# Kernel tuning notes

Hardware: AMD Instinct MI355X
Metric: run time of the kernel (lower is better)

The kernel has to match this reference:

```python
import jax, jax.numpy as jnp
import numpy as np

D = 512      # encoder_dim
DI = 1024    # mamba d_inner = expand * d_model
N = 16       # d_state
DTR = 32     # dt_rank = ceil(512/16)
K = 4        # d_conv
B, L = 8, 512


def _ln(x, g, b, eps=1e-5):
    m = jnp.mean(x, -1, keepdims=True)
    v = jnp.mean((x - m) ** 2, -1, keepdims=True)
    return (x - m) / jnp.sqrt(v + eps) * g + b


def _silu(x):
    return x * jax.nn.sigmoid(x)


def _ffn(x, g, b, w1, b1, w2, b2):
    h = _ln(x, g, b)
    h = _silu(h @ w1.T + b1)
    return h @ w2.T + b2


def _dwconv(x, w, pl, pr):
    # x: (B,C,L); w: (C,K) depthwise kernel
    return jax.lax.conv_general_dilated(
        x, w[:, None, :], (1,), [(pl, pr)],
        feature_group_count=x.shape[1], dimension_numbers=('NCH', 'OIH', 'NCH'))


def _mamba(x, win, convw, convb, wx, wdt, bdt, Alog, Dp, wout):
    b = x.shape[0]
    xz = jnp.einsum('bld,ed->ble', x, win)            # (B,L,2*DI)
    xi, z = jnp.split(xz, 2, -1)
    xc = _dwconv(xi.transpose(0, 2, 1), convw, K - 1, 0) + convb[None, :, None]
    xc = _silu(xc).transpose(0, 2, 1)                 # (B,L,DI) causal conv + silu
    xdb = jnp.einsum('bld,ed->ble', xc, wx)           # (B,L,DTR+2N)
    dt, Bm, Cm = xdb[..., :DTR], xdb[..., DTR:DTR + N], xdb[..., DTR + N:]
    dt = jax.nn.softplus(jnp.einsum('blr,dr->bld', dt, wdt) + bdt)
    A = -jnp.exp(Alog)                                # (DI,N)
    dA = jnp.exp(dt[..., None] * A)                   # (B,L,DI,N)
    dBx = dt[..., None] * Bm[:, :, None, :] * xc[..., None]

    def step(h, t):
        dA_t, dBx_t, C_t = t
        h = dA_t * h + dBx_t
        return h, jnp.einsum('bdn,bn->bd', h, C_t)

    h0 = jnp.zeros((b, DI, N), x.dtype)
    _, ys = jax.lax.scan(step, h0, (dA.transpose(1, 0, 2, 3),
                                    dBx.transpose(1, 0, 2, 3),
                                    Cm.transpose(1, 0, 2)))
    y = ys.transpose(1, 0, 2) + Dp * xc
    y = y * _silu(z)
    return jnp.einsum('bld,od->blo', y, wout)


def _bimamba(x, m_win, m_convw, m_convb, m_wx, m_wdt, m_bdt, m_Alog, m_D, m_wout, bi_wo, bi_bo):
    f = _mamba(x, m_win[0], m_convw[0], m_convb[0], m_wx[0], m_wdt[0], m_bdt[0],
               m_Alog[0], m_D[0], m_wout[0])
    r = _mamba(x[:, ::-1], m_win[1], m_convw[1], m_convb[1], m_wx[1], m_wdt[1], m_bdt[1],
               m_Alog[1], m_D[1], m_wout[1])
    cat = jnp.concatenate([f, r[:, ::-1]], -1)
    return cat @ bi_wo.T + bi_bo


def _convmod(x, ln_g, ln_b, pw1_w, pw1_b, dw15, dw31, dw63,
             bn_g, bn_b, bn_m, bn_v, pw2_w, pw2_b):
    h = _ln(x, ln_g, ln_b).transpose(0, 2, 1)          # (B,D,L)
    h = jnp.einsum('bcl,oc->bol', h, pw1_w) + pw1_b[None, :, None]
    a, g = jnp.split(h, 2, 1)
    h = a * jax.nn.sigmoid(g)                          # GLU on channel dim
    outs = [_dwconv(h, w, (w.shape[-1] - 1) // 2, (w.shape[-1] - 1) // 2)
            for w in (dw15, dw31, dw63)]
    out = (outs[0] + outs[1] + outs[2]) / 3.0          # merge_mode='avg'
    out = (out - bn_m[None, :, None]) / jnp.sqrt(bn_v[None, :, None] + 1e-5) \
          * bn_g[None, :, None] + bn_b[None, :, None]
    out = _silu(out)
    out = jnp.einsum('bcl,oc->bol', out, pw2_w) + pw2_b[None, :, None]
    return out.transpose(0, 2, 1)


def setup_inputs() -> dict:
    key = jax.random.key(0)
    ks = iter(jax.random.split(key, 64))
    def w(*shape, s=0.02):
        return jax.random.normal(next(ks), shape, jnp.float32) * s
    inp = {}
    inp['x'] = jax.random.normal(next(ks), (B, L, D), jnp.float32)
    for p in ('ff1', 'ff2'):
        inp[p + '_ln_g'] = jnp.ones((D,), jnp.float32)
        inp[p + '_ln_b'] = jnp.zeros((D,), jnp.float32)
        inp[p + '_w1'] = w(4 * D, D)
        inp[p + '_b1'] = jnp.zeros((4 * D,), jnp.float32)
        inp[p + '_w2'] = w(D, 4 * D)
        inp[p + '_b2'] = jnp.zeros((D,), jnp.float32)
    inp['m_win'] = w(2, 2 * DI, D)
    inp['m_convw'] = w(2, DI, K, s=0.1)
    inp['m_convb'] = jnp.zeros((2, DI), jnp.float32)
    inp['m_wx'] = w(2, DTR + 2 * N, DI)
    inp['m_wdt'] = w(2, DI, DTR, s=0.1)
    inp['m_bdt'] = jnp.full((2, DI), float(np.log(np.expm1(0.01))), jnp.float32)
    inp['m_Alog'] = jnp.log(jnp.tile(jnp.arange(1, N + 1, dtype=jnp.float32), (2, DI, 1)))
    inp['m_D'] = jnp.ones((2, DI), jnp.float32)
    inp['m_wout'] = w(2, D, DI)
    inp['bi_wo'] = w(D, 2 * D)
    inp['bi_bo'] = jnp.zeros((D,), jnp.float32)
    inp['cv_ln_g'] = jnp.ones((D,), jnp.float32)
    inp['cv_ln_b'] = jnp.zeros((D,), jnp.float32)
    inp['cv_pw1_w'] = w(2 * D, D)
    inp['cv_pw1_b'] = jnp.zeros((2 * D,), jnp.float32)
    inp['cv_dw15'] = w(D, 15, s=0.1)
    inp['cv_dw31'] = w(D, 31, s=0.1)
    inp['cv_dw63'] = w(D, 63, s=0.1)
    inp['cv_bn_g'] = jnp.ones((D,), jnp.float32)
    inp['cv_bn_b'] = jnp.zeros((D,), jnp.float32)
    inp['cv_bn_m'] = jnp.zeros((D,), jnp.float32)
    inp['cv_bn_v'] = jnp.ones((D,), jnp.float32)
    inp['cv_pw2_w'] = w(D, D)
    inp['cv_pw2_b'] = jnp.zeros((D,), jnp.float32)
    inp['ln_g'] = jnp.ones((D,), jnp.float32)
    inp['ln_b'] = jnp.zeros((D,), jnp.float32)
    return inp


def reference(x, ff1_ln_g, ff1_ln_b, ff1_w1, ff1_b1, ff1_w2, ff1_b2,
              ff2_ln_g, ff2_ln_b, ff2_w1, ff2_b1, ff2_w2, ff2_b2,
              m_win, m_convw, m_convb, m_wx, m_wdt, m_bdt, m_Alog, m_D, m_wout,
              bi_wo, bi_bo,
              cv_ln_g, cv_ln_b, cv_pw1_w, cv_pw1_b, cv_dw15, cv_dw31, cv_dw63,
              cv_bn_g, cv_bn_b, cv_bn_m, cv_bn_v, cv_pw2_w, cv_pw2_b,
              ln_g, ln_b):
    h = x + 0.5 * _ffn(x, ff1_ln_g, ff1_ln_b, ff1_w1, ff1_b1, ff1_w2, ff1_b2)
    h = h + _bimamba(h, m_win, m_convw, m_convb, m_wx, m_wdt, m_bdt,
                     m_Alog, m_D, m_wout, bi_wo, bi_bo)
    h = h + _convmod(h, cv_ln_g, cv_ln_b, cv_pw1_w, cv_pw1_b, cv_dw15, cv_dw31, cv_dw63,
                     cv_bn_g, cv_bn_b, cv_bn_m, cv_bn_v, cv_pw2_w, cv_pw2_b)
    h = h + 0.5 * _ffn(h, ff2_ln_g, ff2_ln_b, ff2_w1, ff2_b1, ff2_w2, ff2_b2)
    return _ln(h, ln_g, ln_b)
```

## Files before the change

kernel.cpp:

```cpp
#include <hip/hip_runtime.h>
#include <hip/hip_bf16.h>
#include <math.h>

#define LL   512
#define DD   512
#define DII  1024
#define NST  16
#define BB   8
#define MM   4096
#define CHL  32
#define NCH  16
#define MB_  (1024*1024)
#define Q_(n) ((size_t)(n)*262144)

typedef __attribute__((ext_vector_type(8))) short bf16x8;
typedef __attribute__((ext_vector_type(4))) float f32x4;

__device__ __forceinline__ float fast_rcp(float x){ return __builtin_amdgcn_rcpf(x); }
__device__ __forceinline__ float sigmoidf_(float x){ return fast_rcp(1.0f + __expf(-x)); }
__device__ __forceinline__ float siluf_(float x){ return x * sigmoidf_(x); }
__device__ __forceinline__ float softplusf_(float x){
    return fmaxf(x, 0.0f) + __logf(1.0f + __expf(-fabsf(x)));
}

__device__ __forceinline__ short f2bf(float f) {
    union { float f; unsigned u; } v; v.f = f;
    unsigned r = v.u + 0x7fffu + ((v.u >> 16) & 1u);
    return (short)(r >> 16);
}
__device__ __forceinline__ float bf2f(short s) {
    union { unsigned u; float f; } v; v.u = ((unsigned)(unsigned short)s) << 16;
    return v.f;
}
__device__ __forceinline__ bf16x8 pack_bf8(float4 v0, float4 v1) {
    union { bf16x8 v; short e[8]; } pk;
    pk.e[0]=f2bf(v0.x); pk.e[1]=f2bf(v0.y); pk.e[2]=f2bf(v0.z); pk.e[3]=f2bf(v0.w);
    pk.e[4]=f2bf(v1.x); pk.e[5]=f2bf(v1.y); pk.e[6]=f2bf(v1.z); pk.e[7]=f2bf(v1.w);
    return pk.v;
}
__device__ __forceinline__ void gl_lds16(const short* g, short* l) {
    __builtin_amdgcn_global_load_lds(
        (const __attribute__((address_space(1))) void*)g,
        (__attribute__((address_space(3))) void*)l, 16, 0, 0);
}

struct WcvtArgs { const float* s[10]; short* d[10]; int n[10]; };
__global__ void __launch_bounds__(256) wcvt_kernel(WcvtArgs a) {
    const int seg = blockIdx.y;
    const int i = (blockIdx.x*256 + threadIdx.x) * 8;
    if (i >= a.n[seg]) return;
    const float* s = a.s[seg] + i;
    float4 v0 = *(const float4*)s;
    float4 v1 = *(const float4*)(s + 4);
    int di = i;
    if (seg == 8) di = ((i >> 5) << 6) | (i & 31);
    *(bf16x8*)(a.d[seg] + di) = pack_bf8(v0, v1);
}

__global__ void __launch_bounds__(256) woutT_kernel(
    const float* __restrict__ wout, short* __restrict__ outT)
{
    __shared__ float sh[64][65];
    const int o0 = blockIdx.x << 6;
    const int j0 = blockIdx.y << 6;
    const int d  = blockIdx.z;
    const float* in = wout + (size_t)d*512*1024;
    short* out = outT + (size_t)d*1024*512;
    const int t = threadIdx.x;
    const int c4 = (t & 15) << 2;
    const int r  = t >> 4;
    #pragma unroll
    for (int i = 0; i < 4; i++) {
        int orow = r + i*16;
        float4 v = *(const float4*)(in + (size_t)(o0 + orow)*1024 + j0 + c4);
        sh[orow][c4+0]=v.x; sh[orow][c4+1]=v.y; sh[orow][c4+2]=v.z; sh[orow][c4+3]=v.w;
    }
    __syncthreads();
    #pragma unroll
    for (int i = 0; i < 4; i++) {
        int jr = r + i*16;
        short4 o;
        o.x = f2bf(sh[c4+0][jr]); o.y = f2bf(sh[c4+1][jr]);
        o.z = f2bf(sh[c4+2][jr]); o.w = f2bf(sh[c4+3][jr]);
        *(short4*)(out + (size_t)(j0 + jr)*512 + o0 + c4) = o;
    }
}

__global__ void __launch_bounds__(512) gemm9_kernel(
    const short* __restrict__ A, int lda,
    const short* __restrict__ W, int ldw,
    const float* __restrict__ bias,
    short* __restrict__ outB, int ldc,
    int kLen, int act)
{
    __shared__ short As[3][128*64];
    __shared__ short Ws[3][256*64];

    const int tid = threadIdx.x, lane = tid & 63, wid = tid >> 6;

    int nwg = gridDim.x * gridDim.y;
    int flat = blockIdx.y * gridDim.x + blockIdx.x;
    if (!(nwg & 7)) { int cpx = nwg >> 3; flat = (flat & 7)*cpx + (flat >> 3); }
    const int bx = flat % gridDim.x, by = flat / gridDim.x;
    const int rowBase = by << 7;
    const int colBase = bx << 8;

    size_t asrc[2];
    #pragma unroll
    for (int rd = 0; rd < 2; rd++) {
        int id = rd*512 + tid, row = id >> 3, u = id & 7;
        asrc[rd] = (size_t)(rowBase + row)*lda + ((u ^ (row & 7)) << 3);
    }
    size_t wsrc[4];
    #pragma unroll
    for (int rd = 0; rd < 4; rd++) {
        int id = rd*512 + tid, row = id >> 3, u = id & 7;
        wsrc[rd] = (size_t)(colBase + row)*ldw + ((u ^ (row & 7)) << 3);
    }

    const int fr = lane & 15;
    const int swz0 = ((((lane >> 4)    ) ^ (lane & 7)) << 3);
    const int swz1 = ((((lane >> 4) | 4) ^ (lane & 7)) << 3);
    const int wm = (wid >> 2) * 64, wn = (wid & 3) * 64;

    f32x4 acc[4][4] = {};

    auto STAGE = [&](int buf, int k0) {
        #pragma unroll
        for (int rd = 0; rd < 2; rd++)
            gl_lds16(A + asrc[rd] + k0, &As[buf][(rd*512 + tid)*8]);
        #pragma unroll
        for (int rd = 0; rd < 4; rd++)
            gl_lds16(W + wsrc[rd] + k0, &Ws[buf][(rd*512 + tid)*8]);
    };

    const int nT = kLen >> 6;
    STAGE(0, 0);
    if (nT > 1) STAGE(1, 64);
    for (int t = 0; t < nT; ++t) {
        if (t + 2 < nT) {
            STAGE((t+2)%3, (t+2)*64);
            asm volatile("s_waitcnt vmcnt(12)" ::: "memory");
        } else if (t + 1 < nT) {
            asm volatile("s_waitcnt vmcnt(6)" ::: "memory");
        } else {
            asm volatile("s_waitcnt vmcnt(0)" ::: "memory");
        }
        __builtin_amdgcn_sched_barrier(0);
        __builtin_amdgcn_s_barrier();
        __builtin_amdgcn_sched_barrier(0);
        const int cur = t % 3;
        #pragma unroll
        for (int ks = 0; ks < 2; ks++) {
            const int so = ks ? swz1 : swz0;
            bf16x8 af[4], bfr[4];
            #pragma unroll
            for (int mi = 0; mi < 4; mi++)
                af[mi] = *(const bf16x8*)&As[cur][(wm + mi*16 + fr)*64 + so];
            #pragma unroll
            for (int ni = 0; ni < 4; ni++)
                bfr[ni] = *(const bf16x8*)&Ws[cur][(wn + ni*16 + fr)*64 + so];
            #pragma unroll
            for (int mi = 0; mi < 4; mi++)
                #pragma unroll
                for (int ni = 0; ni < 4; ni++)
                    acc[mi][ni] = __builtin_amdgcn_mfma_f32_16x16x32_bf16(af[mi], bfr[ni], acc[mi][ni], 0, 0, 0);
        }
        __builtin_amdgcn_sched_barrier(0);
        __builtin_amdgcn_s_barrier();
        __builtin_amdgcn_sched_barrier(0);
    }

    #pragma unroll
    for (int mi = 0; mi < 4; mi++)
        #pragma unroll
        for (int r = 0; r < 4; r++) {
            int orow = rowBase + wm + mi*16 + ((lane>>4)<<2) + r;
            #pragma unroll
            for (int ni = 0; ni < 4; ni++) {
                int gcol = colBase + wn + ni*16 + fr;
                float v = acc[mi][ni][r];
                if (bias) v += bias[gcol];
                if (act == 1) v = siluf_(v);
                outB[(size_t)orow*ldc + gcol] = f2bf(v);
            }
        }
}

template<int BN>
__global__ void __launch_bounds__(256) gemm3_kernel(
    const short* __restrict__ A, int lda,
    const short* __restrict__ W, int ldw,
    const float* __restrict__ bias,
    float* __restrict__ outF, short* __restrict__ outB, int ldc,
    int kLen, int kOff, int act, int actLim,
    size_t zA, size_t zW, int zB, size_t zO, int rowsPerW,
    float* __restrict__ partial, size_t pstride, int N)
{
    constexpr int WN = BN / 64;
    constexpr int WM = 4 / WN;
    constexpr int TM = 64 / WM;
    constexpr int FM = TM / 16;
    constexpr int WRW = BN / 32;

    __shared__ short As[2][64*64];
    __shared__ short Ws[2][BN*64];

    const int tid = threadIdx.x, lane = tid & 63, wid = tid >> 6;
    const int z = blockIdx.z;
    A += (size_t)z * zA;
    if (outF) outF += (size_t)z * zO;
    if (outB) outB += (size_t)z * zO;

    int nwg = gridDim.x * gridDim.y;
    int flat = blockIdx.y * gridDim.x + blockIdx.x;
    if (!(nwg & 7)) { int cpx = nwg >> 3; flat = (flat & 7)*cpx + (flat >> 3); }
    const int bx = flat % gridDim.x, by = flat / gridDim.x;

    const int rowBase = by << 6;
    const int colBase = bx * BN;
    const int kBase = z * kOff;

    const int dsel = rowsPerW ? (rowBase / rowsPerW) : z;
    W += (size_t)dsel * zW;
    if (bias) bias += (size_t)dsel * (size_t)zB;

    size_t asrc[2];
    #pragma unroll
    for (int rd = 0; rd < 2; rd++) {
        int id = rd*256 + tid, row = id >> 3, u = id & 7;
        asrc[rd] = (size_t)(rowBase + row)*lda + ((u ^ (row & 7)) << 3);
    }
    size_t wsrc[WRW];
    #pragma unroll
    for (int rd = 0; rd < WRW; rd++) {
        int id = rd*256 + tid, row = id >> 3, u = id & 7;
        wsrc[rd] = (size_t)(colBase + row)*ldw + ((u ^ (row & 7)) << 3);
    }

    const int fr = lane & 15;
    const int swz0 = ((((lane >> 4)    ) ^ (lane & 7)) << 3);
    const int swz1 = ((((lane >> 4) | 4) ^ (lane & 7)) << 3);
    const int wm = (wid / WN) * TM, wn = (wid % WN) * 64;

    f32x4 acc[FM][4] = {};

    auto STAGE = [&](int buf, int k0) {
        #pragma unroll
        for (int rd = 0; rd < 2; rd++)
            gl_lds16(A + asrc[rd] + k0, &As[buf][(rd*256 + tid)*8]);
        #pragma unroll
        for (int rd = 0; rd < WRW; rd++)
            gl_lds16(W + wsrc[rd] + k0, &Ws[buf][(rd*256 + tid)*8]);
    };

    const int nT = kLen >> 6;
    STAGE(0, kBase);
    int cur = 0;
    for (int t = 0; t < nT; ++t) {
        if (t + 1 < nT) {
            STAGE(cur ^ 1, kBase + (t+1)*64);
            asm volatile("s_waitcnt vmcnt(6)" ::: "memory");
        } else {
            asm volatile("s_waitcnt vmcnt(0)" ::: "memory");
        }
        __builtin_amdgcn_sched_barrier(0);
        __builtin_amdgcn_s_barrier();
        __builtin_amdgcn_sched_barrier(0);
        #pragma unroll
        for (int ks = 0; ks < 2; ks++) {
            const int so = ks ? swz1 : swz0;
            bf16x8 af[FM], bfr[4];
            #pragma unroll
            for (int mi = 0; mi < FM; mi++)
                af[mi] = *(const bf16x8*)&As[cur][(wm + mi*16 + fr)*64 + so];
            #pragma unroll
            for (int ni = 0; ni < 4; ni++)
                bfr[ni] = *(const bf16x8*)&Ws[cur][(wn + ni*16 + fr)*64 + so];
            #pragma unroll
            for (int mi = 0; mi < FM; mi++)
                #pragma unroll
                for (int ni = 0; ni < 4; ni++)
                    acc[mi][ni] = __builtin_amdgcn_mfma_f32_16x16x32_bf16(af[mi], bfr[ni], acc[mi][ni], 0, 0, 0);
        }
        __builtin_amdgcn_sched_barrier(0);
        __builtin_amdgcn_s_barrier();
        __builtin_amdgcn_sched_barrier(0);
        cur ^= 1;
    }

    if (partial) {
        float* pp = partial + (size_t)z * pstride;
        #pragma unroll
        for (int mi = 0; mi < FM; mi++)
            #pragma unroll
            for (int r = 0; r < 4; r++) {
                int orow = rowBase + wm + mi*16 + ((lane>>4)<<2) + r;
                #pragma unroll
                for (int ni = 0; ni < 4; ni++)
                    pp[(size_t)orow*N + colBase + wn + ni*16 + fr] = acc[mi][ni][r];
            }
    } else {
        #pragma unroll
        for (int mi = 0; mi < FM; mi++)
            #pragma unroll
            for (int r = 0; r < 4; r++) {
                int orow = rowBase + wm + mi*16 + ((lane>>4)<<2) + r;
                #pragma unroll
                for (int ni = 0; ni < 4; ni++) {
                    int gcol = colBase + wn + ni*16 + fr;
                    float v = acc[mi][ni][r];
                    if (bias) v += bias[gcol];
                    if (gcol < actLim) {
                        if (act == 1) v = siluf_(v);
                        else if (act == 2) v = softplusf_(v);
                    }
                    if (outF) outF[(size_t)orow*ldc + gcol] = v;
                    if (outB) outB[(size_t)orow*ldc + gcol] = f2bf(v);
                }
            }
    }
}

__global__ void __launch_bounds__(256) reduce_kernel(
    const float* __restrict__ part, int S, size_t pstride, int N,
    short* __restrict__ outB, int ldc)
{
    const int i4 = blockIdx.x*256 + threadIdx.x;
    const int row = i4 / (N >> 2);
    const int c4  = (i4 - row*(N >> 2)) << 2;
    float4 s = *(const float4*)(part + (size_t)row*N + c4);
    for (int z = 1; z < S; z++) {
        float4 t = *(const float4*)(part + (size_t)z*pstride + (size_t)row*N + c4);
        s.x += t.x; s.y += t.y; s.z += t.z; s.w += t.w;
    }
    short4 o; o.x=f2bf(s.x); o.y=f2bf(s.y); o.z=f2bf(s.z); o.w=f2bf(s.w);
    *(short4*)(outB + (size_t)row*ldc + c4) = o;
}

__global__ void __launch_bounds__(128) redln_kernel(
    const float* __restrict__ part, int S,
    const float* __restrict__ bias,
    const float* __restrict__ resid, float rscale,
    float* __restrict__ houtF, short* __restrict__ houtB,
    const float* __restrict__ lng, const float* __restrict__ lnb2,
    float* __restrict__ lnoutF, short* __restrict__ lnoutB)
{
    const int row = blockIdx.x;
    const int t = threadIdx.x;
    const size_t pstride = (size_t)MM*512;
    float4 s = ((const float4*)(part + (size_t)row*512))[t];
    for (int z = 1; z < S; z++) {
        float4 v = ((const float4*)(part + z*pstride + (size_t)row*512))[t];
        s.x += v.x; s.y += v.y; s.z += v.z; s.w += v.w;
    }
    if (bias) { float4 b = ((const float4*)bias)[t]; s.x+=b.x; s.y+=b.y; s.z+=b.z; s.w+=b.w; }
    if (resid) {
        float4 r = ((const float4*)(resid + (size_t)row*512))[t];
        s.x = r.x + rscale*s.x; s.y = r.y + rscale*s.y;
        s.z = r.z + rscale*s.z; s.w = r.w + rscale*s.w;
    }
    if (houtF) ((float4*)(houtF + (size_t)row*512))[t] = s;
    if (houtB) {
        short4 o; o.x=f2bf(s.x); o.y=f2bf(s.y); o.z=f2bf(s.z); o.w=f2bf(s.w);
        *(short4*)(houtB + (size_t)row*512 + t*4) = o;
    }
    if (!lng) return;
    float sum = s.x+s.y+s.z+s.w;
    float sq  = s.x*s.x+s.y*s.y+s.z*s.z+s.w*s.w;
    #pragma unroll
    for (int off = 32; off >= 1; off >>= 1) {
        sum += __shfl_down(sum, off);
        sq  += __shfl_down(sq, off);
    }
    __shared__ float sh[4];
    if ((t & 63) == 0) { sh[(t>>6)*2] = sum; sh[(t>>6)*2+1] = sq; }
    __syncthreads();
    float mean = (sh[0]+sh[2]) * (1.0f/512.f);
    float var  = (sh[1]+sh[3]) * (1.0f/512.f) - mean*mean;
    float rstd = rsqrtf(var + 1e-5f);
    float4 gg = ((const float4*)lng)[t];
    float4 bb = ((const float4*)lnb2)[t];
    float4 o;
    o.x = (s.x-mean)*rstd*gg.x + bb.x;
    o.y = (s.y-mean)*rstd*gg.y + bb.y;
    o.z = (s.z-mean)*rstd*gg.z + bb.z;
    o.w = (s.w-mean)*rstd*gg.w + bb.w;
    if (lnoutF) ((float4*)(lnoutF + (size_t)row*512))[t] = o;
    if (lnoutB) {
        short4 ob; ob.x=f2bf(o.x); ob.y=f2bf(o.y); ob.z=f2bf(o.z); ob.w=f2bf(o.w);
        *(short4*)(lnoutB + (size_t)row*512 + t*4) = ob;
    }
}

__global__ void __launch_bounds__(128) ln_kernel(
    const float* __restrict__ x, const float* __restrict__ g,
    const float* __restrict__ bta, short* __restrict__ outB)
{
    const int row = blockIdx.x;
    const int t = threadIdx.x;
    float4 v = ((const float4*)(x + (size_t)row*DD))[t];
    float s = v.x+v.y+v.z+v.w;
    float q = v.x*v.x+v.y*v.y+v.z*v.z+v.w*v.w;
    #pragma unroll
    for (int off = 32; off >= 1; off >>= 1) {
        s += __shfl_down(s, off);
        q += __shfl_down(q, off);
    }
    __shared__ float sh[4];
    if ((t & 63) == 0) { sh[(t>>6)*2] = s; sh[(t>>6)*2+1] = q; }
    __syncthreads();
    float mean = (sh[0]+sh[2]) * (1.0f/DD);
    float var  = (sh[1]+sh[3]) * (1.0f/DD) - mean*mean;
    float rstd = rsqrtf(var + 1e-5f);
    float4 gg = ((const float4*)g)[t];
    float4 bb = ((const float4*)bta)[t];
    short4 ob;
    ob.x = f2bf((v.x-mean)*rstd*gg.x + bb.x);
    ob.y = f2bf((v.y-mean)*rstd*gg.y + bb.y);
    ob.z = f2bf((v.z-mean)*rstd*gg.z + bb.z);
    ob.w = f2bf((v.w-mean)*rstd*gg.w + bb.w);
    *(short4*)(outB + (size_t)row*DD + t*4) = ob;
}

__global__ void __launch_bounds__(256) conv_both_kernel(
    const short* __restrict__ xz_all, const float* __restrict__ cw,
    const float* __restrict__ cb, short* __restrict__ xc_both)
{
    const int gid = blockIdx.x*256 + threadIdx.x;
    const int c4  = (gid & 255) << 2;
    const int row = (gid >> 8) & (MM-1);
    const int dir = gid >> 20;
    const int l   = row & (LL-1);
    const short* base = xz_all + (size_t)(row - l)*4096 + dir*2048 + c4;
    float acc[4];
    #pragma unroll
    for (int j = 0; j < 4; j++) acc[j] = cb[dir*1024 + c4 + j];
    float wt[4][4];
    #pragma unroll
    for (int j = 0; j < 4; j++) {
        float4 w = *(const float4*)(cw + (size_t)dir*4096 + (c4 + j)*4);
        wt[j][0]=w.x; wt[j][1]=w.y; wt[j][2]=w.z; wt[j][3]=w.w;
    }
    #pragma unroll
    for (int t = 0; t < 4; t++) {
        int lt = dir ? (l + 3 - t) : (l - 3 + t);
        if (lt >= 0 && lt < LL) {
            short4 u = *(const short4*)(base + (size_t)lt*4096);
            acc[0] += wt[0][t]*bf2f(u.x);
            acc[1] += wt[1][t]*bf2f(u.y);
            acc[2] += wt[2][t]*bf2f(u.z);
            acc[3] += wt[3][t]*bf2f(u.w);
        }
    }
    short4 o;
    o.x = f2bf(siluf_(acc[0])); o.y = f2bf(siluf_(acc[1]));
    o.z = f2bf(siluf_(acc[2])); o.w = f2bf(siluf_(acc[3]));
    *(short4*)(xc_both + (size_t)dir*MM*1024 + (size_t)row*1024 + c4) = o;
}

__global__ void __launch_bounds__(256) scan_a_kernel(
    const short* __restrict__ dt_bf, const short* __restrict__ xc_both,
    const short* __restrict__ xdb_bf, const float* __restrict__ Alog,
    float* __restrict__ S_dt, short* __restrict__ H)
{
    const int bid = blockIdx.x;
    const int dg  = bid & 3;
    const int c   = (bid >> 2) & (NCH-1);
    const int b   = (bid >> 6) & 7;
    const int dir = bid >> 9;
    const int d   = (dg << 8) + threadIdx.x;

    float Aexp[16];
    #pragma unroll
    for (int n = 0; n < 16; n++) Aexp[n] = -__expf(Alog[dir*16384 + d*16 + n]);
    const float A0 = Aexp[0];
    int fast = 1;
    #pragma unroll
    for (int n = 1; n < 16; n++)
        fast &= (fabsf(Aexp[n] - (float)(n+1)*A0) <= 1e-4f*fabsf(Aexp[n]) + 1e-6f);

    float h[16];
    #pragma unroll
    for (int n = 0; n < 16; n++) h[n] = 0.f;
    float S = 0.f;

    const size_t rbase = (size_t)b*LL + (size_t)c*CHL;
    const short* dtp = dt_bf + ((size_t)dir*MM + rbase)*1024 + d;
    const short* bcp = xdb_bf + ((size_t)dir*MM + rbase)*64 + 32;
    const short* xcp = xc_both + ((size_t)dir*MM + rbase)*1024 + d;

#define SCAN_A_BODY(FASTQ) \
    for (int i = 0; i < CHL; i++) { \
        int lp = dir ? (CHL-1-i) : i; \
        float dtv = bf2f(dtp[(size_t)lp*1024]); \
        float xcv = bf2f(xcp[(size_t)lp*1024]); \
        S += dtv; \
        float co = dtv*xcv; \
        union { bf16x8 v; short e[8]; } b0, b1; \
        b0.v = *(const bf16x8*)(bcp + (size_t)lp*64); \
        b1.v = *(const bf16x8*)(bcp + (size_t)lp*64 + 8); \
        float q[16]; \
        if (FASTQ) { \
            float p = __expf(dtv*A0); float qq = p; \
            _Pragma("unroll") for (int n = 0; n < 16; n++) { q[n] = qq; qq *= p; } \
        } else { \
            _Pragma("unroll") for (int n = 0; n < 16; n++) q[n] = __expf(dtv*Aexp[n]); \
        } \
        _Pragma("unroll") for (int n = 0; n < 16; n++) { \
            float Bv = bf2f(n < 8 ? b0.e[n] : b1.e[n & 7]); \
            h[n] = fmaf(q[n], h[n], co*Bv); \
        } \
    }
    if (fast) { SCAN_A_BODY(1) } else { SCAN_A_BODY(0) }
#undef SCAN_A_BODY

    S_dt[(((size_t)dir*BB + b)*NCH + c)*1024 + d] = S;
    const size_t hb = ((((size_t)dir*BB + b)*NCH + c)*16)*1024 + d;
    #pragma unroll
    for (int n = 0; n < 16; n++) H[hb + (size_t)n*1024] = f2bf(h[n]);
}

__global__ void __launch_bounds__(256) scan_b_kernel(
    const float* __restrict__ S_dt, short* H, const float* __restrict__ Alog)
{
    const int g = blockIdx.x*256 + threadIdx.x;
    const int d = g & 1023;
    const int n = (g >> 10) & 15;
    const int b = (g >> 14) & 7;
    const int dir = g >> 17;
    const float Aexp = -__expf(Alog[dir*16384 + d*16 + n]);
    float h = 0.f;
    for (int ci = 0; ci < NCH; ci++) {
        int c = dir ? (NCH-1-ci) : ci;
        float S = S_dt[(((size_t)dir*BB + b)*NCH + c)*1024 + d];
        size_t i = ((((size_t)dir*BB + b)*NCH + c)*16 + n)*1024 + d;
        float q = __expf(Aexp*S);
        float hn = q*h + bf2f(H[i]);
        H[i] = f2bf(h);
        h = hn;
    }
}

__global__ void __launch_bounds__(256) scan_c_kernel(
    const short* __restrict__ dt_bf, short* xc_ys,
    const short* __restrict__ xdb_bf, const float* __restrict__ Alog,
    const short* __restrict__ H, const short* __restrict__ xz_all,
    const float* __restrict__ Dp)
{
    const int bid = blockIdx.x;
    const int dg  = bid & 3;
    const int c   = (bid >> 2) & (NCH-1);
    const int b   = (bid >> 6) & 7;
    const int dir = bid >> 9;
    const int d   = (dg << 8) + threadIdx.x;

    float Aexp[16];
    #pragma unroll
    for (int n = 0; n < 16; n++) Aexp[n] = -__expf(Alog[dir*16384 + d*16 + n]);
    const float A0 = Aexp[0];
    int fast = 1;
    #pragma unroll
    for (int n = 1; n < 16; n++)
        fast &= (fabsf(Aexp[n] - (float)(n+1)*A0) <= 1e-4f*fabsf(Aexp[n]) + 1e-6f);
    const float Dpv = Dp[dir*1024 + d];

    float h[16];
    const size_t hb = ((((size_t)dir*BB + b)*NCH + c)*16)*1024 + d;
    #pragma unroll
    for (int n = 0; n < 16; n++) h[n] = bf2f(H[hb + (size_t)n*1024]);

    const size_t rbase = (size_t)b*LL + (size_t)c*CHL;
    const short* dtp = dt_bf + ((size_t)dir*MM + rbase)*1024 + d;
    const short* bcp = xdb_bf + ((size_t)dir*MM + rbase)*64 + 32;
    short*       xcp = xc_ys + ((size_t)dir*MM + rbase)*1024 + d;
    const short* zp  = xz_all + rbase*4096 + dir*2048 + 1024 + d;

#define SCAN_C_BODY(FASTQ) \
    for (int i = 0; i < CHL; i++) { \
        int lp = dir ? (CHL-1-i) : i; \
        float dtv = bf2f(dtp[(size_t)lp*1024]); \
        float xcv = bf2f(xcp[(size_t)lp*1024]); \
        float zv  = bf2f(zp[(size_t)lp*4096]); \
        float co = dtv*xcv; \
        union { bf16x8 v; short e[8]; } b0, b1, c0, c1; \
        b0.v = *(const bf16x8*)(bcp + (size_t)lp*64); \
        b1.v = *(const bf16x8*)(bcp + (size_t)lp*64 + 8); \
        c0.v = *(const bf16x8*)(bcp + (size_t)lp*64 + 16); \
        c1.v = *(const bf16x8*)(bcp + (size_t)lp*64 + 24); \
        float q[16]; \
        if (FASTQ) { \
            float p = __expf(dtv*A0); float qq = p; \
            _Pragma("unroll") for (int n = 0; n < 16; n++) { q[n] = qq; qq *= p; } \
        } else { \
            _Pragma("unroll") for (int n = 0; n < 16; n++) q[n] = __expf(dtv*Aexp[n]); \
        } \
        float y = 0.f; \
        _Pragma("unroll") for (int n = 0; n < 16; n++) { \
            float Bv = bf2f(n < 8 ? b0.e[n] : b1.e[n & 7]); \
            float Cv = bf2f(n < 8 ? c0.e[n] : c1.e[n & 7]); \
            h[n] = fmaf(q[n], h[n], co*Bv); \
            y = fmaf(Cv, h[n], y); \
        } \
        float out = (y + Dpv*xcv) * siluf_(zv); \
        xcp[(size_t)lp*1024] = f2bf(out); \
    }
    if (fast) { SCAN_C_BODY(1) } else { SCAN_C_BODY(0) }
#undef SCAN_C_BODY
}

__global__ void __launch_bounds__(256) glu_transpose_kernel(
    const float* __restrict__ pw1, float* __restrict__ out_t)
{
    __shared__ float sh[64][65];
    const int c0 = blockIdx.x << 6;
    const int l0 = blockIdx.y << 6;
    const int b  = blockIdx.z;
    const int t  = threadIdx.x;
    const int c4 = (t & 15) << 2;
    const int r  = t >> 4;
    #pragma unroll
    for (int i = 0; i < 4; i++) {
        int lrow = r + i*16;
        size_t row = (size_t)(b << 9) + l0 + lrow;
        float4 a = *(const float4*)(pw1 + row*1024 + c0 + c4);
        float4 g = *(const float4*)(pw1 + row*1024 + 512 + c0 + c4);
        sh[lrow][c4+0] = a.x * sigmoidf_(g.x);
        sh[lrow][c4+1] = a.y * sigmoidf_(g.y);
        sh[lrow][c4+2] = a.z * sigmoidf_(g.z);
        sh[lrow][c4+3] = a.w * sigmoidf_(g.w);
    }
    __syncthreads();
    #pragma unroll
    for (int i = 0; i < 4; i++) {
        int crow = r + i*16;
        float4 o;
        o.x = sh[c4+0][crow];
        o.y = sh[c4+1][crow];
        o.z = sh[c4+2][crow];
        o.w = sh[c4+3][crow];
        *(float4*)(out_t + ((size_t)(b << 9) + c0 + crow)*512 + l0 + c4) = o;
    }
}

__global__ void __launch_bounds__(256) multiconv_t_kernel(
    const float* __restrict__ gin_t,
    const float* __restrict__ w15, const float* __restrict__ w31,
    const float* __restrict__ w63,
    const float* __restrict__ bn_g, const float* __restrict__ bn_b,
    const float* __restrict__ bn_m, const float* __restrict__ bn_v,
    float* __restrict__ out_t)
{
    __shared__ float sh[574];
    const int c = blockIdx.x & (DD-1);
    const int b = blockIdx.x >> 9;
    const int t = threadIdx.x;
    const float* rowp = gin_t + ((size_t)(b << 9) + c)*512;
    sh[31 + t]       = rowp[t];
    sh[31 + t + 256] = rowp[t + 256];
    if (t < 31) { sh[t] = 0.f; sh[543 + t] = 0.f; }
    __syncthreads();

    const float bnscale = rsqrtf(bn_v[c] + 1e-5f) * bn_g[c];
    const float bnm = bn_m[c], bnb = bn_b[c];
    float* outp = out_t + ((size_t)(b << 9) + c)*512;
    #pragma unroll
    for (int half = 0; half < 2; half++) {
        int l = t + half*256;
        float s63 = 0.f, s31 = 0.f, s15 = 0.f;
        #pragma unroll
        for (int k = 0; k < 63; k++) s63 += w63[c*63 + k] * sh[l + k];
        #pragma unroll
        for (int k = 0; k < 31; k++) s31 += w31[c*31 + k] * sh[l + 16 + k];
        #pragma unroll
        for (int k = 0; k < 15; k++) s15 += w15[c*15 + k] * sh[l + 24 + k];
        float m = (s15 + s31 + s63) * (1.0f/3.0f);
        m = (m - bnm) * bnscale + bnb;
        outp[l] = siluf_(m);
    }
}

__global__ void __launch_bounds__(256) transpose_bcl_kernel(
    const float* __restrict__ in_t, short* __restrict__ out)
{
    __shared__ float sh[64][65];
    const int l0 = blockIdx.x << 6;
    const int c0 = blockIdx.y << 6;
    const int b  = blockIdx.z;
    const int t  = threadIdx.x;
    const int l4 = (t & 15) << 2;
    const int r  = t >> 4;
    #pragma unroll
    for (int i = 0; i < 4; i++) {
        int crow = r + i*16;
        float4 v = *(const float4*)(in_t + ((size_t)(b << 9) + c0 + crow)*512 + l0 + l4);
        sh[crow][l4+0] = v.x; sh[crow][l4+1] = v.y;
        sh[crow][l4+2] = v.z; sh[crow][l4+3] = v.w;
    }
    __syncthreads();
    #pragma unroll
    for (int i = 0; i < 4; i++) {
        int lrow = r + i*16;
        short4 o;
        o.x = f2bf(sh[l4+0][lrow]);
        o.y = f2bf(sh[l4+1][lrow]);
        o.z = f2bf(sh[l4+2][lrow]);
        o.w = f2bf(sh[l4+3][lrow]);
        *(short4*)(out + ((size_t)(b << 9) + l0 + lrow)*512 + c0 + l4) = o;
    }
}

extern "C" void kernel_launch(void* const* d_in, const int* in_sizes, int n_in,
                              void* d_out, int out_size, void* d_ws, size_t ws_size,
                              hipStream_t stream)
{
    const float* x        = (const float*)d_in[0];
    const float* ff1_ln_g = (const float*)d_in[1];
    const float* ff1_ln_b = (const float*)d_in[2];
    const float* ff1_w1   = (const float*)d_in[3];
    const float* ff1_b1   = (const float*)d_in[4];
    const float* ff1_w2   = (const float*)d_in[5];
    const float* ff1_b2   = (const float*)d_in[6];
    const float* ff2_ln_g = (const float*)d_in[7];
    const float* ff2_ln_b = (const float*)d_in[8];
    const float* ff2_w1   = (const float*)d_in[9];
    const float* ff2_b1   = (const float*)d_in[10];
    const float* ff2_w2   = (const float*)d_in[11];
    const float* ff2_b2   = (const float*)d_in[12];
    const float* m_win    = (const float*)d_in[13];
    const float* m_convw  = (const float*)d_in[14];
    const float* m_convb  = (const float*)d_in[15];
    const float* m_wx     = (const float*)d_in[16];
    const float* m_wdt    = (const float*)d_in[17];
    const float* m_bdt    = (const float*)d_in[18];
    const float* m_Alog   = (const float*)d_in[19];
    const float* m_Dp     = (const float*)d_in[20];
    const float* m_wout   = (const float*)d_in[21];
    const float* bi_wo    = (const float*)d_in[22];
    const float* bi_bo    = (const float*)d_in[23];
    const float* cv_ln_g  = (const float*)d_in[24];
    const float* cv_ln_b  = (const float*)d_in[25];
    const float* cv_pw1_w = (const float*)d_in[26];
    const float* cv_pw1_b = (const float*)d_in[27];
    const float* cv_dw15  = (const float*)d_in[28];
    const float* cv_dw31  = (const float*)d_in[29];
    const float* cv_dw63  = (const float*)d_in[30];
    const float* cv_bn_g  = (const float*)d_in[31];
    const float* cv_bn_b  = (const float*)d_in[32];
    const float* cv_bn_m  = (const float*)d_in[33];
    const float* cv_bn_v  = (const float*)d_in[34];
    const float* cv_pw2_w = (const float*)d_in[35];
    const float* cv_pw2_b = (const float*)d_in[36];
    const float* ln_g     = (const float*)d_in[37];
    const float* ln_b     = (const float*)d_in[38];

    char* wsb = (char*)d_ws;
    float* h        = (float*)(wsb + Q_(0));
    short* h_bf     = (short*)(wsb + Q_(32));
    short* lnb_bf   = (short*)(wsb + Q_(48));
    short* w_ff1w1  = (short*)(wsb + Q_(64));
    short* w_ff1w2  = (short*)(wsb + Q_(72));
    short* w_ff2w1  = (short*)(wsb + Q_(80));
    short* w_ff2w2  = (short*)(wsb + Q_(88));
    short* w_win    = (short*)(wsb + Q_(96));
    short* w_pw1    = (short*)(wsb + Q_(112));
    short* w_pw2    = (short*)(wsb + Q_(116));
    short* w_Wc     = (short*)(wsb + Q_(118));
    short* w_wdtp   = (short*)(wsb + Q_(126));
    short* w_wx     = (short*)(wsb + Q_(127));
    float* part     = (float*)(wsb + Q_(128));
    short* Hbuf     = (short*)(wsb + Q_(128));
    float* S_dt     = (float*)(wsb + Q_(192));
    short* xz_all   = (short*)(wsb + Q_(226));
    short* woutT_ov = (short*)(wsb + Q_(226));
    short* biwo_ov  = (short*)(wsb + Q_(234));
    float* glu_t    = (float*)(wsb + Q_(226));
    short* xc_both  = (short*)(wsb + Q_(290));
    short* hid_bf   = (short*)(wsb + Q_(290));
    short* dt_bf    = (short*)(wsb + Q_(354));
    float* mconv_o  = (float*)(wsb + Q_(354));
    short* xdb_bf   = (short*)(wsb + Q_(418));

    if (ws_size < Q_(422)) return;

    hipMemsetAsync(w_wdtp, 0, (size_t)2*1024*64*2, stream);
    WcvtArgs wa;
    wa.s[0]=ff1_w1;   wa.d[0]=w_ff1w1; wa.n[0]=1048576;
    wa.s[1]=ff1_w2;   wa.d[1]=w_ff1w2; wa.n[1]=1048576;
    wa.s[2]=ff2_w1;   wa.d[2]=w_ff2w1; wa.n[2]=1048576;
    wa.s[3]=ff2_w2;   wa.d[3]=w_ff2w2; wa.n[3]=1048576;
    wa.s[4]=m_win;    wa.d[4]=w_win;   wa.n[4]=2097152;
    wa.s[5]=bi_wo;    wa.d[5]=biwo_ov; wa.n[5]=524288;
    wa.s[6]=cv_pw1_w; wa.d[6]=w_pw1;   wa.n[6]=524288;
    wa.s[7]=cv_pw2_w; wa.d[7]=w_pw2;   wa.n[7]=262144;
    wa.s[8]=m_wdt;    wa.d[8]=w_wdtp;  wa.n[8]=65536;
    wa.s[9]=m_wx;     wa.d[9]=w_wx;    wa.n[9]=131072;
    wcvt_kernel<<<dim3(1024,10), 256, 0, stream>>>(wa);
    woutT_kernel<<<dim3(8,16,2), 256, 0, stream>>>(m_wout, woutT_ov);

    auto G = [&](const short* A, int lda, const short* W, int ldw,
                 const float* bias, float* oF, short* oB, int ldc,
                 int M, int N, int nz, int kLen, int kOff,
                 size_t zA, size_t zW, int zB, size_t zO, int rowsPerW,
                 int act, int actLim, float* prt) {
        dim3 g(N/128, M/64, nz);
        gemm3_kernel<128><<<g, 256, 0, stream>>>(A, lda, W, ldw, bias, oF, oB, ldc,
            kLen, kOff, act, actLim, zA, zW, zB, zO, rowsPerW,
            prt, (size_t)M*N, N);
    };

    G(biwo_ov, 1024, woutT_ov, 512, nullptr, nullptr, w_Wc, 1024,
      512, 1024, 2, 512, 0, 512, 524288, 0, 524288, 0, 0, 0, nullptr);

    ln_kernel<<<MM, 128, 0, stream>>>(x, ff1_ln_g, ff1_ln_b, lnb_bf);
    gemm9_kernel<<<dim3(8, 32), 512, 0, stream>>>(lnb_bf, 512, w_ff1w1, 512,
        ff1_b1, hid_bf, 2048, 512, 1);
    G(hid_bf, 2048, w_ff1w2, 2048, nullptr, nullptr, nullptr, 0,
      MM, 512, 2, 1024, 1024, 0, 0, 0, 0, 0, 0, 0, part);
    redln_kernel<<<MM, 128, 0, stream>>>(part, 2, ff1_b2, x, 0.5f,
        h, h_bf, nullptr, nullptr, nullptr, nullptr);

    gemm9_kernel<<<dim3(16, 32), 512, 0, stream>>>(h_bf, 512, w_win, 512,
        nullptr, xz_all, 4096, 512, 0);
    conv_both_kernel<<<8192, 256, 0, stream>>>(xz_all, m_convw, m_convb, xc_both);
    {
        dim3 g(1, 128, 4);
        gemm3_kernel<64><<<g, 256, 0, stream>>>(xc_both, 1024, w_wx, 1024,
            nullptr, nullptr, nullptr, 0, 256, 256, 0, 0,
            0, 65536, 0, 0, 4096, part, (size_t)8192*64, 64);
    }
    reduce_kernel<<<512, 256, 0, stream>>>(part, 4, (size_t)8192*64, 64, xdb_bf, 64);
    G(xdb_bf, 64, w_wdtp, 64, m_bdt, nullptr, dt_bf, 1024,
      8192, 1024, 1, 64, 0, 0, 65536, 1024, 0, 4096, 2, 1024, nullptr);
    scan_a_kernel<<<1024, 256, 0, stream>>>(dt_bf, xc_both, xdb_bf, m_Alog, S_dt, Hbuf);
    scan_b_kernel<<<1024, 256, 0, stream>>>(S_dt, Hbuf, m_Alog);
    scan_c_kernel<<<1024, 256, 0, stream>>>(dt_bf, xc_both, xdb_bf, m_Alog, Hbuf,
                                            xz_all, m_Dp);
    G(xc_both, 1024, w_Wc, 1024, nullptr, nullptr, nullptr, 0,
      MM, 512, 2, 1024, 0, (size_t)MM*1024, 524288, 0, 0, 0, 0, 0, part);
    redln_kernel<<<MM, 128, 0, stream>>>(part, 2, bi_bo, h, 1.0f,
        h, nullptr, cv_ln_g, cv_ln_b, nullptr, lnb_bf);

    G(lnb_bf, 512, w_pw1, 512, cv_pw1_b, part, nullptr, 1024,
      MM, 1024, 1, 512, 0, 0, 0, 0, 0, 0, 0, 0, nullptr);
    glu_transpose_kernel<<<dim3(8,8,8), 256, 0, stream>>>(part, glu_t);
    multiconv_t_kernel<<<BB*DD, 256, 0, stream>>>(glu_t,
        cv_dw15, cv_dw31, cv_dw63, cv_bn_g, cv_bn_b, cv_bn_m, cv_bn_v, mconv_o);
    transpose_bcl_kernel<<<dim3(8,8,8), 256, 0, stream>>>(mconv_o, lnb_bf);
    G(lnb_bf, 512, w_pw2, 512, nullptr, nullptr, nullptr, 0,
      MM, 512, 2, 256, 256, 0, 0, 0, 0, 0, 0, 0, part);
    redln_kernel<<<MM, 128, 0, stream>>>(part, 2, cv_pw2_b, h, 1.0f,
        h, nullptr, ff2_ln_g, ff2_ln_b, nullptr, lnb_bf);

    gemm9_kernel<<<dim3(8, 32), 512, 0, stream>>>(lnb_bf, 512, w_ff2w1, 512,
        ff2_b1, hid_bf, 2048, 512, 1);
    G(hid_bf, 2048, w_ff2w2, 2048, nullptr, nullptr, nullptr, 0,
      MM, 512, 2, 1024, 1024, 0, 0, 0, 0, 0, 0, 0, part);
    redln_kernel<<<MM, 128, 0, stream>>>(part, 2, ff2_b2, h, 0.5f,
        nullptr, nullptr, ln_g, ln_b, (float*)d_out, nullptr);
}
```

Baseline: 373.6 us.

## Fuse residual add into GEMM epilogue and drop split-K for FFN/pw2

Adds a residual-add epilogue (resid + scale*v) to the generic GEMM and uses it for the FFN1 second matmul, conv pw2, and FFN2 second matmul. These GEMMs now run with a single K split instead of two, writing final residual sums directly rather than fp32 partials. The separate partial-sum reduction and residual work disappears, and where a following LayerNorm is still needed, redln only normalizes. The trade-off is half as many blocks for these 4096x512 GEMMs with longer K loops, which lowers parallelism on a large GPU. Some steps also compute in place with h serving as both residual input and output.

```diff
diff --git a/kernel.cpp b/kernel.cpp
--- a/kernel.cpp
+++ b/kernel.cpp
@@ -193,6 +193,7 @@
     const short* __restrict__ W, int ldw,
     const float* __restrict__ bias,
     float* __restrict__ outF, short* __restrict__ outB, int ldc,
+    const float* __restrict__ resid, int ldr, float rscale,
     int kLen, int kOff, int act, int actLim,
     size_t zA, size_t zW, int zB, size_t zO, int rowsPerW,
     float* __restrict__ partial, size_t pstride, int N)
@@ -315,6 +316,7 @@
                         if (act == 1) v = siluf_(v);
                         else if (act == 2) v = softplusf_(v);
                     }
+                    if (resid) v = resid[(size_t)orow*ldr + gcol] + rscale*v;
                     if (outF) outF[(size_t)orow*ldc + gcol] = v;
                     if (outB) outB[(size_t)orow*ldc + gcol] = f2bf(v);
                 }
@@ -800,25 +802,24 @@
 
     auto G = [&](const short* A, int lda, const short* W, int ldw,
                  const float* bias, float* oF, short* oB, int ldc,
+                 const float* res, int ldr, float rs,
                  int M, int N, int nz, int kLen, int kOff,
                  size_t zA, size_t zW, int zB, size_t zO, int rowsPerW,
                  int act, int actLim, float* prt) {
         dim3 g(N/128, M/64, nz);
         gemm3_kernel<128><<<g, 256, 0, stream>>>(A, lda, W, ldw, bias, oF, oB, ldc,
-            kLen, kOff, act, actLim, zA, zW, zB, zO, rowsPerW,
+            res, ldr, rs, kLen, kOff, act, actLim, zA, zW, zB, zO, rowsPerW,
             prt, (size_t)M*N, N);
     };
 
     G(biwo_ov, 1024, woutT_ov, 512, nullptr, nullptr, w_Wc, 1024,
-      512, 1024, 2, 512, 0, 512, 524288, 0, 524288, 0, 0, 0, nullptr);
+      nullptr, 0, 0.f, 512, 1024, 2, 512, 0, 512, 524288, 0, 524288, 0, 0, 0, nullptr);
 
     ln_kernel<<<MM, 128, 0, stream>>>(x, ff1_ln_g, ff1_ln_b, lnb_bf);
     gemm9_kernel<<<dim3(8, 32), 512, 0, stream>>>(lnb_bf, 512, w_ff1w1, 512,
         ff1_b1, hid_bf, 2048, 512, 1);
-    G(hid_bf, 2048, w_ff1w2, 2048, nullptr, nullptr, nullptr, 0,
-      MM, 512, 2, 1024, 1024, 0, 0, 0, 0, 0, 0, 0, part);
-    redln_kernel<<<MM, 128, 0, stream>>>(part, 2, ff1_b2, x, 0.5f,
-        h, h_bf, nullptr, nullptr, nullptr, nullptr);
+    G(hid_bf, 2048, w_ff1w2, 2048, ff1_b2, h, h_bf, 512,
+      x, 512, 0.5f, MM, 512, 1, 2048, 0, 0, 0, 0, 0, 0, 0, 0, nullptr);
 
     gemm9_kernel<<<dim3(16, 32), 512, 0, stream>>>(h_bf, 512, w_win, 512,
         nullptr, xz_all, 4096, 512, 0);
@@ -826,36 +827,36 @@
     {
         dim3 g(1, 128, 4);
         gemm3_kernel<64><<<g, 256, 0, stream>>>(xc_both, 1024, w_wx, 1024,
-            nullptr, nullptr, nullptr, 0, 256, 256, 0, 0,
+            nullptr, nullptr, nullptr, 0, nullptr, 0, 0.f, 256, 256, 0, 0,
             0, 65536, 0, 0, 4096, part, (size_t)8192*64, 64);
     }
     reduce_kernel<<<512, 256, 0, stream>>>(part, 4, (size_t)8192*64, 64, xdb_bf, 64);
     G(xdb_bf, 64, w_wdtp, 64, m_bdt, nullptr, dt_bf, 1024,
-      8192, 1024, 1, 64, 0, 0, 65536, 1024, 0, 4096, 2, 1024, nullptr);
+      nullptr, 0, 0.f, 8192, 1024, 1, 64, 0, 0, 65536, 1024, 0, 4096, 2, 1024, nullptr);
     scan_a_kernel<<<1024, 256, 0, stream>>>(dt_bf, xc_both, xdb_bf, m_Alog, S_dt, Hbuf);
     scan_b_kernel<<<1024, 256, 0, stream>>>(S_dt, Hbuf, m_Alog);
     scan_c_kernel<<<1024, 256, 0, stream>>>(dt_bf, xc_both, xdb_bf, m_Alog, Hbuf,
                                             xz_all, m_Dp);
     G(xc_both, 1024, w_Wc, 1024, nullptr, nullptr, nullptr, 0,
-      MM, 512, 2, 1024, 0, (size_t)MM*1024, 524288, 0, 0, 0, 0, 0, part);
+      nullptr, 0, 0.f, MM, 512, 2, 1024, 0, (size_t)MM*1024, 524288, 0, 0, 0, 0, 0, part);
     redln_kernel<<<MM, 128, 0, stream>>>(part, 2, bi_bo, h, 1.0f,
         h, nullptr, cv_ln_g, cv_ln_b, nullptr, lnb_bf);
 
     G(lnb_bf, 512, w_pw1, 512, cv_pw1_b, part, nullptr, 1024,
-      MM, 1024, 1, 512, 0, 0, 0, 0, 0, 0, 0, 0, nullptr);
+      nullptr, 0, 0.f, MM, 1024, 1, 512, 0, 0, 0, 0, 0, 0, 0, 0, nullptr);
     glu_transpose_kernel<<<dim3(8,8,8), 256, 0, stream>>>(part, glu_t);
     multiconv_t_kernel<<<BB*DD, 256, 0, stream>>>(glu_t,
         cv_dw15, cv_dw31, cv_dw63, cv_bn_g, cv_bn_b, cv_bn_m, cv_bn_v, mconv_o);
     transpose_bcl_kernel<<<dim3(8,8,8), 256, 0, stream>>>(mconv_o, lnb_bf);
-    G(lnb_bf, 512, w_pw2, 512, nullptr, nullptr, nullptr, 0,
-      MM, 512, 2, 256, 256, 0, 0, 0, 0, 0, 0, 0, part);
-    redln_kernel<<<MM, 128, 0, stream>>>(part, 2, cv_pw2_b, h, 1.0f,
-        h, nullptr, ff2_ln_g, ff2_ln_b, nullptr, lnb_bf);
+    G(lnb_bf, 512, w_pw2, 512, cv_pw2_b, h, nullptr, 512,
+      h, 512, 1.0f, MM, 512, 1, 512, 0, 0, 0, 0, 0, 0, 0, 0, nullptr);
+    redln_kernel<<<MM, 128, 0, stream>>>(h, 1, nullptr, nullptr, 0.f,
+        nullptr, nullptr, ff2_ln_g, ff2_ln_b, nullptr, lnb_bf);
 
     gemm9_kernel<<<dim3(8, 32), 512, 0, stream>>>(lnb_bf, 512, w_ff2w1, 512,
         ff2_b1, hid_bf, 2048, 512, 1);
-    G(hid_bf, 2048, w_ff2w2, 2048, nullptr, nullptr, nullptr, 0,
-      MM, 512, 2, 1024, 1024, 0, 0, 0, 0, 0, 0, 0, part);
-    redln_kernel<<<MM, 128, 0, stream>>>(part, 2, ff2_b2, h, 0.5f,
+    G(hid_bf, 2048, w_ff2w2, 2048, ff2_b2, h, nullptr, 512,
+      h, 512, 0.5f, MM, 512, 1, 2048, 0, 0, 0, 0, 0, 0, 0, 0, nullptr);
+    redln_kernel<<<MM, 128, 0, stream>>>(h, 1, nullptr, nullptr, 0.f,
         nullptr, nullptr, ln_g, ln_b, (float*)d_out, nullptr);
 }
```

Measured after the change: 421.3 us. 12.8% more time.
